# Performance work log

Hardware: AMD Instinct MI355X
Metric: run time of the kernel (lower is better)

## Reference

```python
import jax, jax.numpy as jnp
import numpy as np

NUM_HEADS = 4
IN_CHANNELS = 128


def setup_inputs() -> dict:
    key = jax.random.key(0)
    k_x, k_wq, k_bq, k_wo, k_bo = jax.random.split(key, 5)
    b, c, h, w = 16, IN_CHANNELS, 32, 32
    x = jax.random.normal(k_x, (b, c, h, w), dtype=jnp.float32)
    # 1x1 convs stored as (out_ch, in_ch) matrices
    w_qkv = jax.random.normal(k_wq, (c * 3 * NUM_HEADS, c), dtype=jnp.float32) * 0.02
    b_qkv = jax.random.normal(k_bq, (c * 3 * NUM_HEADS,), dtype=jnp.float32) * 0.02
    w_out = jax.random.normal(k_wo, (c, c * NUM_HEADS), dtype=jnp.float32) * 0.02
    b_out = jax.random.normal(k_bo, (c,), dtype=jnp.float32) * 0.02
    return {"x": x, "w_qkv": w_qkv, "b_qkv": b_qkv, "w_out": w_out, "b_out": b_out}


def reference(x, w_qkv, b_qkv, w_out, b_out):
    b, c, h, w = x.shape
    nh = NUM_HEADS
    # norm is Identity. 1x1 conv == per-pixel matmul over channels.
    qkv = jnp.einsum('bchw,oc->bohw', x, w_qkv) + b_qkv[None, :, None, None]
    qkv = qkv.reshape(b, nh, 3 * c, h, w)
    q, k, v = qkv[:, :, :c], qkv[:, :, c:2 * c], qkv[:, :, 2 * c:]
    # q, v: (b, nh, c, h, w) -> (b*nh, h*w, c); k -> (b*nh, c, h*w)
    q = q.transpose(0, 1, 3, 4, 2).reshape(b * nh, h * w, c)
    k = k.reshape(b * nh, c, h * w)
    v = v.transpose(0, 1, 3, 4, 2).reshape(b * nh, h * w, c)
    scores = jnp.einsum('bnc,bcm->bnm', q, k) * (c ** -0.5)  # (b*nh, hw, hw)
    attn = jax.nn.softmax(scores, axis=-1)
    out = jnp.einsum('bnm,bmc->bnc', attn, v)  # (b*nh, hw, c)
    out = out.reshape(b, nh, h, w, c).transpose(0, 4, 1, 2, 3).reshape(b, nh * c, h, w)
    out = jnp.einsum('bchw,oc->bohw', out, w_out) + b_out[None, :, None, None]
    return out + x
```

## Files before the change

### kernel.cpp

```cpp
#include <hip/hip_runtime.h>
#include <hip/hip_bf16.h>

typedef float  f32x4_v   __attribute__((ext_vector_type(4)));
typedef float  f32x16_v  __attribute__((ext_vector_type(16)));
typedef __bf16 bf16x8_v  __attribute__((ext_vector_type(8)));
typedef __bf16 bf16x4_v  __attribute__((ext_vector_type(4)));

#define WS_Q  0
#define WS_K  8388608
#define WS_V  16777216
#define WS_O  25165824
#define WS_WP 33554432

__device__ __forceinline__ int aswz(int p) { return ((p & 7) ^ ((p >> 3) & 7)) << 4; }

__device__ __forceinline__ void gload16(const void* g, void* l) {
    __builtin_amdgcn_global_load_lds(
        (const __attribute__((address_space(1))) unsigned int*)g,
        (__attribute__((address_space(3))) unsigned int*)l, 16, 0, 0);
}

__global__ __launch_bounds__(256) void k_qkv(const float* __restrict__ x,
                                             const float* __restrict__ w_qkv,
                                             const float* __restrict__ b_qkv,
                                             __bf16* __restrict__ q_ws,
                                             __bf16* __restrict__ k_ws,
                                             __bf16* __restrict__ v_ws,
                                             const float* __restrict__ w_out,
                                             __bf16* __restrict__ w_perm) {
    __shared__ __bf16 Ash[128 * 128];
    __shared__ __bf16 Bsh[128 * 128];
    const int tid  = threadIdx.x;
    const int quar = blockIdx.x;
    const int mt   = blockIdx.y;
    const int gm0  = mt * 128;
    const int b    = gm0 >> 10;
    const int p0   = gm0 & 1023;

    if (quar < 2) {
        int gid  = (mt * 2 + quar) * 256 + tid;
        int head = gid >> 14;
        int o    = (gid >> 7) & 127;
        int c    = gid & 127;
        w_perm[gid] = (__bf16)w_out[o * 512 + c * 4 + head];
    }

    char* Ab = reinterpret_cast<char*>(Ash);
    char* Bb = reinterpret_cast<char*>(Bsh);

    for (int it = 0; it < 16; ++it) {
        int idx = tid + it * 256;
        int c   = idx >> 5;
        int i4  = (idx & 31) << 2;
        float4 v = *reinterpret_cast<const float4*>(x + b * 131072 + c * 1024 + p0 + i4);
        float vv[4] = {v.x, v.y, v.z, v.w};
#pragma unroll
        for (int j = 0; j < 4; ++j) {
            int p = i4 + j;
            int byte = ((p << 8) | (c << 1)) ^ aswz(p);
            *reinterpret_cast<__bf16*>(Ab + byte) = (__bf16)vv[j];
        }
    }

    const int lane = tid & 63;
    const int wv   = tid >> 6;
    const int wm   = (wv >> 1) * 64;
    const int wn   = (wv & 1) * 64;
    const int lr   = lane & 15;
    const int lg   = lane >> 4;

    for (int i = 0; i < 3; ++i) {
        const int o0 = (quar * 3 + i) * 128;
        __syncthreads();
        for (int it = 0; it < 16; ++it) {
            int idx = tid + it * 256;
            int o   = idx >> 5;
            int c4  = (idx & 31) << 2;
            float4 v = *reinterpret_cast<const float4*>(w_qkv + (o0 + o) * 128 + c4);
            bf16x4_v h;
            h[0] = (__bf16)v.x; h[1] = (__bf16)v.y; h[2] = (__bf16)v.z; h[3] = (__bf16)v.w;
            int byte = ((o << 8) | (c4 << 1)) ^ aswz(o);
            *reinterpret_cast<bf16x4_v*>(Bb + byte) = h;
        }
        __syncthreads();

        f32x4_v acc[4][4] = {};
#pragma unroll
        for (int ks = 0; ks < 4; ++ks) {
            bf16x8_v af[4], bfr[4];
#pragma unroll
            for (int mi = 0; mi < 4; ++mi) {
                int row  = wm + mi * 16 + lr;
                int byte = ((row << 8) | (ks << 6) | (lg << 4)) ^ aswz(row);
                af[mi] = *reinterpret_cast<const bf16x8_v*>(Ab + byte);
            }
#pragma unroll
            for (int ni = 0; ni < 4; ++ni) {
                int row  = wn + ni * 16 + lr;
                int byte = ((row << 8) | (ks << 6) | (lg << 4)) ^ aswz(row);
                bfr[ni] = *reinterpret_cast<const bf16x8_v*>(Bb + byte);
            }
#pragma unroll
            for (int mi = 0; mi < 4; ++mi)
#pragma unroll
                for (int ni = 0; ni < 4; ++ni)
                    acc[mi][ni] = __builtin_amdgcn_mfma_f32_16x16x32_bf16(af[mi], bfr[ni], acc[mi][ni], 0, 0, 0);
        }

#pragma unroll
        for (int ni = 0; ni < 4; ++ni) {
            int o    = o0 + wn + ni * 16 + lr;
            int head = o / 384;
            int rem  = o - head * 384;
            int type = rem >> 7;
            int ch   = rem & 127;
            float bias = b_qkv[o];
            int bh   = (b << 2) + head;
            int ksd  = ch >> 4;
            int hid  = (ch >> 3) & 1;
            int ed   = ch & 7;
#pragma unroll
            for (int mi = 0; mi < 4; ++mi) {
                int prow = p0 + wm + mi * 16 + lg * 4;
                f32x4_v a = acc[mi][ni];
                if (type == 0) {
#pragma unroll
                    for (int r = 0; r < 4; ++r) {
                        int q = prow + r;
                        q_ws[bh * 131072 + (q >> 5) * 4096 + ksd * 512 + hid * 256 + (q & 31) * 8 + ed] =
                            (__bf16)((a[r] + bias) * 0.12751744f);
                    }
                } else if (type == 1) {
#pragma unroll
                    for (int r = 0; r < 4; ++r) {
                        int kv = prow + r;
                        k_ws[bh * 131072 + (kv >> 5) * 4096 + ksd * 512 + hid * 256 + (kv & 31) * 8 + ed] =
                            (__bf16)(a[r] + bias);
                    }
                } else {
                    bf16x4_v hv;
#pragma unroll
                    for (int r = 0; r < 4; ++r) hv[r] = (__bf16)(a[r] + bias);
                    int addr = bh * 131072 + (prow >> 5) * 4096 +
                               ((ch >> 5) * 2 + ((prow >> 4) & 1)) * 512 +
                               ((prow >> 3) & 1) * 256 + (ch & 31) * 8 + (prow & 7);
                    *reinterpret_cast<bf16x4_v*>(&v_ws[addr]) = hv;
                }
            }
        }
    }
}

__global__ __launch_bounds__(256, 2) void k_attn(const __bf16* __restrict__ q_ws,
                                                 const __bf16* __restrict__ k_ws,
                                                 const __bf16* __restrict__ v_ws,
                                                 __bf16* __restrict__ o_ws) {
    __shared__ __bf16 Kbuf[2][8192];

    const int tid  = threadIdx.x;
    const int lane = tid & 63;
    const int wv   = tid >> 6;
    const int col  = lane & 31;
    const int hi   = lane >> 5;

    const int id   = blockIdx.x;
    const int bh   = (id & 7) * 8 + (id >> 6);
    const int qt   = (id >> 3) & 7;
    const int base = bh * 131072;
    const int q0w  = qt * 128 + wv * 32;

    const char* kfb = reinterpret_cast<const char*>(k_ws + base);
    const uint64_t vfb = (uint64_t)reinterpret_cast<const char*>(v_ws + base) + lane * 16;
    const int lane16 = lane * 16;

#pragma unroll
    for (int i = 0; i < 4; ++i)
        gload16(kfb + (wv * 4 + i) * 1024 + lane16, (char*)&Kbuf[0][0] + (wv * 4 + i) * 1024);

    bf16x8_v bq[8];
    {
        const __bf16* qp = q_ws + base + (q0w >> 5) * 4096 + lane * 8;
#pragma unroll
        for (int ks = 0; ks < 8; ++ks)
            bq[ks] = *reinterpret_cast<const bf16x8_v*>(qp + ks * 512);
    }
    asm volatile("s_waitcnt vmcnt(0)" ::: "memory");

    f32x16_v of[4] = {};
    float l = 0.f;
    bf16x8_v vf[4][4];

#pragma unroll
    for (int n = 0; n < 4; ++n) {
        uint64_t va0 = vfb + (uint64_t)(n * 2048);
        uint64_t va1 = va0 + 8192;
        asm volatile("global_load_dwordx4 %0, %4, off\n\t"
                     "global_load_dwordx4 %1, %4, off offset:1024\n\t"
                     "global_load_dwordx4 %2, %5, off\n\t"
                     "global_load_dwordx4 %3, %5, off offset:1024"
                     : "=&v"(vf[n][0]), "=&v"(vf[n][1]), "=&v"(vf[n][2]), "=&v"(vf[n][3])
                     : "v"(va0), "v"(va1));
    }

    for (int t = 0; t < 16; ++t) {
        const int cur = t & 1;
        const char* Kl = (const char*)&Kbuf[cur][0];

        __builtin_amdgcn_s_barrier();
        asm volatile("" ::: "memory");
        __builtin_amdgcn_sched_barrier(0);

        if (t < 15) {
            const char* kn = kfb + (t + 1) * 16384;
            char* dn = (char*)&Kbuf[cur ^ 1][0];
#pragma unroll
            for (int i = 0; i < 4; ++i)
                gload16(kn + (wv * 4 + i) * 1024 + lane16, dn + (wv * 4 + i) * 1024);
            asm volatile("s_waitcnt vmcnt(20)" ::: "memory");
        } else {
            asm volatile("s_waitcnt vmcnt(16)" ::: "memory");
        }
        __builtin_amdgcn_sched_barrier(0);

        f32x16_v sa = {}, sb = {};
        __builtin_amdgcn_s_setprio(1);
#pragma unroll
        for (int ks = 0; ks < 8; ++ks) {
            bf16x8_v af0 = *reinterpret_cast<const bf16x8_v*>(Kl + ks * 1024 + lane16);
            bf16x8_v af1 = *reinterpret_cast<const bf16x8_v*>(Kl + (8 + ks) * 1024 + lane16);
            sa = __builtin_amdgcn_mfma_f32_32x32x16_bf16(af0, bq[ks], sa, 0, 0, 0);
            sb = __builtin_amdgcn_mfma_f32_32x32x16_bf16(af1, bq[ks], sb, 0, 0, 0);
        }
        __builtin_amdgcn_s_setprio(0);

        asm volatile("s_waitcnt lgkmcnt(0)" ::: "memory");
        __builtin_amdgcn_sched_barrier(0);

        float rs = 0.f;
#pragma unroll
        for (int r = 0; r < 16; ++r) { sa[r] = __builtin_amdgcn_exp2f(sa[r]); rs += sa[r]; }
#pragma unroll
        for (int r = 0; r < 16; ++r) { sb[r] = __builtin_amdgcn_exp2f(sb[r]); rs += sb[r]; }
        l += rs + __shfl_xor(rs, 32);

        bf16x8_v pa[4];
#pragma unroll
        for (int j = 0; j < 4; ++j) {
            const f32x16_v& sj = (j < 2) ? sa : sb;
            const int ro = 8 * (j & 1);
            unsigned w0, w1, w2, w3;
            asm("v_cvt_pk_bf16_f32 %0, %1, %2" : "=v"(w0) : "v"(sj[ro + 0]), "v"(sj[ro + 1]));
            asm("v_cvt_pk_bf16_f32 %0, %1, %2" : "=v"(w2) : "v"(sj[ro + 4]), "v"(sj[ro + 5]));
            asm("v_cvt_pk_bf16_f32 %0, %1, %2" : "=v"(w1) : "v"(sj[ro + 2]), "v"(sj[ro + 3]));
            asm("v_cvt_pk_bf16_f32 %0, %1, %2" : "=v"(w3) : "v"(sj[ro + 6]), "v"(sj[ro + 7]));
            asm("v_permlane32_swap_b32 %0, %1" : "+v"(w0), "+v"(w2));
            asm("v_permlane32_swap_b32 %0, %1" : "+v"(w1), "+v"(w3));
            union { unsigned u[4]; bf16x8_v h; } cvt;
            cvt.u[0] = w0; cvt.u[1] = w1; cvt.u[2] = w2; cvt.u[3] = w3;
            pa[j] = cvt.h;
        }

        if (t < 15) asm volatile("s_waitcnt vmcnt(4)" ::: "memory");
        else        asm volatile("s_waitcnt vmcnt(0)" ::: "memory");
        __builtin_amdgcn_sched_barrier(0);

        __builtin_amdgcn_s_setprio(1);
#pragma unroll
        for (int n = 0; n < 4; ++n) {
#pragma unroll
            for (int j = 0; j < 4; ++j)
                of[n] = __builtin_amdgcn_mfma_f32_32x32x16_bf16(pa[j], vf[n][j], of[n], 0, 0, 0);
            if (t < 15) {
                uint64_t va0 = vfb + (uint64_t)((t + 1) * 16384) + (uint64_t)(n * 2048);
                uint64_t va1 = va0 + 8192;
                asm volatile("global_load_dwordx4 %0, %4, off\n\t"
                             "global_load_dwordx4 %1, %4, off offset:1024\n\t"
                             "global_load_dwordx4 %2, %5, off\n\t"
                             "global_load_dwordx4 %3, %5, off offset:1024"
                             : "=&v"(vf[n][0]), "=&v"(vf[n][1]), "=&v"(vf[n][2]), "=&v"(vf[n][3])
                             : "v"(va0), "v"(va1));
            }
        }
        __builtin_amdgcn_s_setprio(0);
    }

    float linv = 1.0f / l;
#pragma unroll
    for (int r = 0; r < 16; ++r) {
        int qr = (r & 3) + 4 * hi + 8 * (r >> 2);
        float ld = __shfl(linv, qr);
        int qg = q0w + qr;
#pragma unroll
        for (int n = 0; n < 4; ++n)
            o_ws[base + qg * 128 + 32 * n + col] = (__bf16)(of[n][r] * ld);
    }
}

__global__ __launch_bounds__(128) void k_out(const __bf16* __restrict__ o_ws,
                                             const __bf16* __restrict__ w_perm,
                                             const float* __restrict__ b_out,
                                             const float* __restrict__ x,
                                             float* __restrict__ out) {
    __shared__ __bf16 Al[32 * 136];
    __shared__ __bf16 Bl[128 * 136];
    const int tid  = threadIdx.x;
    const int lane = tid & 63, wv = tid >> 6;
    const int lr   = lane & 15, lg = lane >> 4;
    const int mt   = blockIdx.x;
    const int gp0  = mt * 32;
    const int b    = gp0 >> 10;
    const int p0   = gp0 & 1023;

    f32x4_v acc[8] = {};
    for (int kc = 0; kc < 4; ++kc) {
        __syncthreads();
#pragma unroll
        for (int it = 0; it < 4; ++it) {
            int idx = tid + it * 128;
            int rr = idx >> 4, k8 = (idx & 15) * 8;
            *reinterpret_cast<bf16x8_v*>(&Al[rr * 136 + k8]) =
                *reinterpret_cast<const bf16x8_v*>(&o_ws[(b * 4 + kc) * 131072 + (p0 + rr) * 128 + k8]);
        }
#pragma unroll
        for (int it = 0; it < 16; ++it) {
            int idx = tid + it * 128;
            int o = idx >> 4, k8 = (idx & 15) * 8;
            *reinterpret_cast<bf16x8_v*>(&Bl[o * 136 + k8]) =
                *reinterpret_cast<const bf16x8_v*>(&w_perm[kc * 16384 + o * 128 + k8]);
        }
        __syncthreads();
#pragma unroll
        for (int ks = 0; ks < 4; ++ks) {
            bf16x8_v af = *reinterpret_cast<const bf16x8_v*>(&Al[(wv * 16 + lr) * 136 + ks * 32 + lg * 8]);
#pragma unroll
            for (int ni = 0; ni < 8; ++ni) {
                bf16x8_v bf_ = *reinterpret_cast<const bf16x8_v*>(&Bl[(ni * 16 + lr) * 136 + ks * 32 + lg * 8]);
                acc[ni] = __builtin_amdgcn_mfma_f32_16x16x32_bf16(af, bf_, acc[ni], 0, 0, 0);
            }
        }
    }

    int prow = p0 + wv * 16 + lg * 4;
#pragma unroll
    for (int ni = 0; ni < 8; ++ni) {
        int o = ni * 16 + lr;
        float bias = b_out[o];
        float4 xr = *reinterpret_cast<const float4*>(&x[b * 131072 + o * 1024 + prow]);
        float4 res;
        res.x = acc[ni][0] + bias + xr.x;
        res.y = acc[ni][1] + bias + xr.y;
        res.z = acc[ni][2] + bias + xr.z;
        res.w = acc[ni][3] + bias + xr.w;
        *reinterpret_cast<float4*>(&out[b * 131072 + o * 1024 + prow]) = res;
    }
}

extern "C" void kernel_launch(void* const* d_in, const int* in_sizes, int n_in,
                              void* d_out, int out_size, void* d_ws, size_t ws_size,
                              hipStream_t stream) {
    const float* x     = (const float*)d_in[0];
    const float* w_qkv = (const float*)d_in[1];
    const float* b_qkv = (const float*)d_in[2];
    const float* w_out = (const float*)d_in[3];
    const float* b_out = (const float*)d_in[4];
    float* out = (float*)d_out;
    __bf16* ws = (__bf16*)d_ws;

    __bf16* q_ws   = ws + WS_Q;
    __bf16* k_ws   = ws + WS_K;
    __bf16* v_ws   = ws + WS_V;
    __bf16* o_ws   = ws + WS_O;
    __bf16* w_perm = ws + WS_WP;

    k_qkv<<<dim3(4, 128), 256, 0, stream>>>(x, w_qkv, b_qkv, q_ws, k_ws, v_ws, w_out, w_perm);
    k_attn<<<512, 256, 0, stream>>>(q_ws, k_ws, v_ws, o_ws);
    k_out<<<512, 128, 0, stream>>>(o_ws, w_perm, b_out, x, out);
}
```

Measured before the change: 83.49 us.

## Stage V tiles through double-buffered LDS instead of per-wave register loads

V tiles were loaded from global memory straight into registers by every wave, so all four waves fetched the same V data. They are now loaded into a shared double-buffered LDS buffer with global_load_lds alongside K, and the wait counts are adjusted to match. Each block fetches V once and the V register array is freed. The cost is 32KB more LDS, which may limit occupancy, plus LDS reads that now sit on the PV MFMA path.

```diff
diff --git a/kernel.cpp b/kernel.cpp
--- a/kernel.cpp
+++ b/kernel.cpp
@@ -156,6 +156,7 @@
                                                  const __bf16* __restrict__ v_ws,
                                                  __bf16* __restrict__ o_ws) {
     __shared__ __bf16 Kbuf[2][8192];
+    __shared__ __bf16 Vbuf[2][8192];
 
     const int tid  = threadIdx.x;
     const int lane = tid & 63;
@@ -170,12 +171,15 @@
     const int q0w  = qt * 128 + wv * 32;
 
     const char* kfb = reinterpret_cast<const char*>(k_ws + base);
-    const uint64_t vfb = (uint64_t)reinterpret_cast<const char*>(v_ws + base) + lane * 16;
+    const char* vfb = reinterpret_cast<const char*>(v_ws + base);
     const int lane16 = lane * 16;
 
 #pragma unroll
     for (int i = 0; i < 4; ++i)
         gload16(kfb + (wv * 4 + i) * 1024 + lane16, (char*)&Kbuf[0][0] + (wv * 4 + i) * 1024);
+#pragma unroll
+    for (int i = 0; i < 4; ++i)
+        gload16(vfb + (wv * 4 + i) * 1024 + lane16, (char*)&Vbuf[0][0] + (wv * 4 + i) * 1024);
 
     bf16x8_v bq[8];
     {
@@ -188,23 +192,11 @@
 
     f32x16_v of[4] = {};
     float l = 0.f;
-    bf16x8_v vf[4][4];
-
-#pragma unroll
-    for (int n = 0; n < 4; ++n) {
-        uint64_t va0 = vfb + (uint64_t)(n * 2048);
-        uint64_t va1 = va0 + 8192;
-        asm volatile("global_load_dwordx4 %0, %4, off\n\t"
-                     "global_load_dwordx4 %1, %4, off offset:1024\n\t"
-                     "global_load_dwordx4 %2, %5, off\n\t"
-                     "global_load_dwordx4 %3, %5, off offset:1024"
-                     : "=&v"(vf[n][0]), "=&v"(vf[n][1]), "=&v"(vf[n][2]), "=&v"(vf[n][3])
-                     : "v"(va0), "v"(va1));
-    }
 
     for (int t = 0; t < 16; ++t) {
         const int cur = t & 1;
         const char* Kl = (const char*)&Kbuf[cur][0];
+        const char* Vl = (const char*)&Vbuf[cur][0];
 
         __builtin_amdgcn_s_barrier();
         asm volatile("" ::: "memory");
@@ -212,13 +204,18 @@
 
         if (t < 15) {
             const char* kn = kfb + (t + 1) * 16384;
-            char* dn = (char*)&Kbuf[cur ^ 1][0];
+            const char* vn = vfb + (t + 1) * 16384;
+            char* dk = (char*)&Kbuf[cur ^ 1][0];
+            char* dv = (char*)&Vbuf[cur ^ 1][0];
 #pragma unroll
             for (int i = 0; i < 4; ++i)
-                gload16(kn + (wv * 4 + i) * 1024 + lane16, dn + (wv * 4 + i) * 1024);
-            asm volatile("s_waitcnt vmcnt(20)" ::: "memory");
+                gload16(kn + (wv * 4 + i) * 1024 + lane16, dk + (wv * 4 + i) * 1024);
+#pragma unroll
+            for (int i = 0; i < 4; ++i)
+                gload16(vn + (wv * 4 + i) * 1024 + lane16, dv + (wv * 4 + i) * 1024);
+            asm volatile("s_waitcnt vmcnt(8)" ::: "memory");
         } else {
-            asm volatile("s_waitcnt vmcnt(16)" ::: "memory");
+            asm volatile("s_waitcnt vmcnt(0)" ::: "memory");
         }
         __builtin_amdgcn_sched_barrier(0);
 
@@ -232,9 +229,6 @@
             sb = __builtin_amdgcn_mfma_f32_32x32x16_bf16(af1, bq[ks], sb, 0, 0, 0);
         }
         __builtin_amdgcn_s_setprio(0);
-
-        asm volatile("s_waitcnt lgkmcnt(0)" ::: "memory");
-        __builtin_amdgcn_sched_barrier(0);
 
         float rs = 0.f;
 #pragma unroll
@@ -260,28 +254,20 @@
             pa[j] = cvt.h;
         }
 
-        if (t < 15) asm volatile("s_waitcnt vmcnt(4)" ::: "memory");
-        else        asm volatile("s_waitcnt vmcnt(0)" ::: "memory");
+        __builtin_amdgcn_s_setprio(1);
+#pragma unroll
+        for (int n = 0; n < 4; ++n) {
+#pragma unroll
+            for (int j = 0; j < 4; ++j) {
+                bf16x8_v bv = *reinterpret_cast<const bf16x8_v*>(
+                    Vl + (j >> 1) * 8192 + (n * 2 + (j & 1)) * 1024 + lane16);
+                of[n] = __builtin_amdgcn_mfma_f32_32x32x16_bf16(pa[j], bv, of[n], 0, 0, 0);
+            }
+        }
+        __builtin_amdgcn_s_setprio(0);
+
+        asm volatile("s_waitcnt lgkmcnt(0)" ::: "memory");
         __builtin_amdgcn_sched_barrier(0);
-
-        __builtin_amdgcn_s_setprio(1);
-#pragma unroll
-        for (int n = 0; n < 4; ++n) {
-#pragma unroll
-            for (int j = 0; j < 4; ++j)
-                of[n] = __builtin_amdgcn_mfma_f32_32x32x16_bf16(pa[j], vf[n][j], of[n], 0, 0, 0);
-            if (t < 15) {
-                uint64_t va0 = vfb + (uint64_t)((t + 1) * 16384) + (uint64_t)(n * 2048);
-                uint64_t va1 = va0 + 8192;
-                asm volatile("global_load_dwordx4 %0, %4, off\n\t"
-                             "global_load_dwordx4 %1, %4, off offset:1024\n\t"
-                             "global_load_dwordx4 %2, %5, off\n\t"
-                             "global_load_dwordx4 %3, %5, off offset:1024"
-                             : "=&v"(vf[n][0]), "=&v"(vf[n][1]), "=&v"(vf[n][2]), "=&v"(vf[n][3])
-                             : "v"(va0), "v"(va1));
-            }
-        }
-        __builtin_amdgcn_s_setprio(0);
     }
 
     float linv = 1.0f / l;
```

Measured after the change: 82.37 us. About the same (-1.3%).
